# Kernel optimization log

Hardware: AMD Instinct MI355X
Metric: run time of the kernel (lower is better)

Reference implementation:

```python
import jax, jax.numpy as jnp
import numpy as np
from jax.scipy.linalg import expm

D = 12   # Fock cutoff dimension
M = 4    # qumodes per circuit
L = 2    # CVNN layers
K = M * (M - 1) // 2  # beamsplitters per interferometer
B = 1024

def _lad():
    # annihilation operator a in truncated Fock basis
    return jnp.diag(jnp.sqrt(jnp.arange(1, D, dtype=jnp.float32)), k=1).astype(jnp.complex64)

def _disp_gen(rr, ph):
    # generator of Displacement(r, phi): alpha*adag - conj(alpha)*a
    lad = _lad()
    alpha = (rr * jnp.exp(1j * ph)).astype(jnp.complex64)
    return alpha * lad.conj().T - jnp.conj(alpha) * lad

def _squeeze_mat(rr, ph):
    lad = _lad()
    z = (rr * jnp.exp(1j * ph)).astype(jnp.complex64)
    a2 = lad @ lad
    return expm(0.5 * (jnp.conj(z) * a2 - z * a2.conj().T))

def _rot_diag(ph):
    n = jnp.arange(D, dtype=jnp.float32)
    return jnp.exp(1j * ph * n).astype(jnp.complex64)

def _kerr_diag(kap):
    n = jnp.arange(D, dtype=jnp.float32)
    return jnp.exp(1j * kap * n * n).astype(jnp.complex64)

def _bs_mat(th, ph):
    # Beamsplitter exp(theta*(e^{i phi} a b^dag - e^{-i phi} a^dag b)) on D^2 space
    lad = _lad()
    eye = jnp.eye(D, dtype=jnp.complex64)
    a1 = jnp.kron(lad, eye)
    a2 = jnp.kron(eye, lad)
    H = th * (jnp.exp(1j * ph) * (a1 @ a2.conj().T) - jnp.exp(-1j * ph) * (a1.conj().T @ a2))
    return expm(H.astype(jnp.complex64)).reshape(D, D, D, D)

def _apply_1mode(psi, U, mode):
    psi = jnp.moveaxis(psi, mode + 1, -1)
    psi = psi @ U.T
    return jnp.moveaxis(psi, -1, mode + 1)

def _apply_1mode_batched(psi, U, mode):
    psi = jnp.moveaxis(psi, mode + 1, -1)
    psi = jnp.einsum('bij,b...j->b...i', U, psi)
    return jnp.moveaxis(psi, -1, mode + 1)

def _apply_diag(psi, d, mode):
    shape = [1] * psi.ndim
    shape[mode + 1] = D
    return psi * d.reshape(shape)

def _apply_2mode(psi, G, mode):
    psi = jnp.moveaxis(psi, (mode + 1, mode + 2), (-2, -1))
    psi = jnp.einsum('ijkl,...kl->...ij', G, psi)
    return jnp.moveaxis(psi, (-2, -1), (mode + 1, mode + 2))

def _interferometer(psi, theta, phi, varphi):
    # PennyLane rectangular (Clements) mesh, then per-mode rotations
    n = 0
    for ll in range(M):
        for kk in range(M - 1):
            if (ll + kk) % 2 != 1:
                psi = _apply_2mode(psi, _bs_mat(theta[n], phi[n]), kk)
                n += 1
    for m in range(M):
        psi = _apply_diag(psi, _rot_diag(varphi[m]), m)
    return psi

def _forward(x, theta_1, phi_1, varphi_1, r, phi_r, theta_2, phi_2, varphi_2, a, phi_a, k):
    b = x.shape[0]
    psi = jnp.zeros((b,) + (D,) * M, dtype=jnp.complex64)
    psi = psi.at[(slice(None),) + (0,) * M].set(1.0)  # vacuum
    # Amplitude_Phase encoding: Displacement(x[:, m], x[:, m+M]) on mode m
    for m in range(M):
        U = jax.vmap(lambda rr, ph: expm(_disp_gen(rr, ph)))(x[:, m], x[:, m + M])
        psi = _apply_1mode_batched(psi, U, m)
    # CVNeuralNetLayers
    for l in range(L):
        psi = _interferometer(psi, theta_1[l], phi_1[l], varphi_1[l])
        for m in range(M):
            psi = _apply_1mode(psi, _squeeze_mat(r[l, m], phi_r[l, m]), m)
        psi = _interferometer(psi, theta_2[l], phi_2[l], varphi_2[l])
        for m in range(M):
            psi = _apply_1mode(psi, expm(_disp_gen(a[l, m], phi_a[l, m])), m)
            psi = _apply_diag(psi, _kerr_diag(k[l, m]), m)
    # X-quadrature expvals (SF convention hbar=2: X = a + adag)
    lad = _lad()
    Xmat = lad + lad.conj().T
    sum_axes = tuple(range(1, M + 1))
    outs = [jnp.real(jnp.sum(jnp.conj(psi) * _apply_1mode(psi, Xmat, m), axis=sum_axes)) for m in range(M)]
    return jnp.stack(outs, axis=1)

def setup_inputs():
    key = jax.random.key(0)
    ks = jax.random.split(key, 12)
    tp = 2.0 * np.pi
    return {
        'x': jax.random.normal(ks[0], (B, 2 * M), dtype=jnp.float32),
        'theta_1': tp * jax.random.uniform(ks[1], (L, K), dtype=jnp.float32),
        'phi_1': tp * jax.random.uniform(ks[2], (L, K), dtype=jnp.float32),
        'varphi_1': tp * jax.random.uniform(ks[3], (L, M), dtype=jnp.float32),
        'r': 0.1 * jax.random.uniform(ks[4], (L, M), dtype=jnp.float32),
        'phi_r': tp * jax.random.uniform(ks[5], (L, M), dtype=jnp.float32),
        'theta_2': tp * jax.random.uniform(ks[6], (L, K), dtype=jnp.float32),
        'phi_2': tp * jax.random.uniform(ks[7], (L, K), dtype=jnp.float32),
        'varphi_2': tp * jax.random.uniform(ks[8], (L, M), dtype=jnp.float32),
        'a': 0.1 * jax.random.uniform(ks[9], (L, M), dtype=jnp.float32),
        'phi_a': tp * jax.random.uniform(ks[10], (L, M), dtype=jnp.float32),
        'k': tp * jax.random.uniform(ks[11], (L, M), dtype=jnp.float32),
    }

def reference(x, theta_1, phi_1, varphi_1, r, phi_r, theta_2, phi_2, varphi_2, a, phi_a, k):
    return _forward(x, theta_1, phi_1, varphi_1, r, phi_r, theta_2, phi_2, varphi_2, a, phi_a, k)
```

## Files before the change

### kernel.cpp

```cpp
#include <hip/hip_runtime.h>
#include <math.h>

#define D4 20736
#define ST 14
#define SST 168
#define KP 18

typedef float2 c32;

__device__ __forceinline__ c32 cmul(c32 a, c32 b) {
  return make_float2(a.x * b.x - a.y * b.y, a.x * b.y + a.y * b.x);
}
__device__ __forceinline__ c32 cfma(c32 a, c32 b, c32 acc) {
  acc.x = fmaf(a.x, b.x, fmaf(-a.y, b.y, acc.x));
  acc.y = fmaf(a.x, b.y, fmaf(a.y, b.x, acc.y));
  return acc;
}
__device__ __forceinline__ c32 get2(const float4* w, int n) {
  float4 q = w[n >> 1];
  return (n & 1) ? make_float2(q.z, q.w) : make_float2(q.x, q.y);
}
__device__ __forceinline__ float4 pack2(c32 a, c32 b) {
  return make_float4(a.x, a.y, b.x, b.y);
}
#define CZERO make_float2(0.f, 0.f)

__constant__ int d_secoff[24] = {0,1,5,14,30,55,91,140,204,285,385,506,650,
                                 771,871,952,1016,1065,1101,1126,1142,1151,1155,1156};

struct RM { int goff, sz, a0, da, r0, dr; };
__device__ __forceinline__ RM rmeta(int r) {
  const int i = r / 12, j = r - 12 * i, N = i + j;
  const bool up = (N <= 11);
  RM m;
  m.sz = (up ? N : 22 - N) + 1;
  const int lo = up ? 0 : (N - 11);
  m.goff = d_secoff[N] + (i - lo) * m.sz;
  m.a0 = up ? N : (143 + N);
  m.da = up ? 13 : -13;
  m.r0 = up ? N : (121 + N);
  m.dr = up ? 11 : -11;
  return m;
}

__device__ void small_expm(c32* A, c32* S, c32* P, c32* T, float* red, int sz, int tid) {
  const int n2 = sz * sz;
  if (tid < sz) {
    float s = 0.f;
    for (int j = 0; j < sz; ++j) { c32 v = A[tid * sz + j]; s += sqrtf(fmaf(v.x, v.x, v.y * v.y)); }
    red[tid] = s;
  }
  __syncthreads();
  float nrm = 0.f;
  for (int i = 0; i < sz; ++i) nrm = fmaxf(nrm, red[i]);
  int sp = 0;
  while (nrm > 0.35f && sp < 24) { nrm *= 0.5f; ++sp; }
  const float scale = ldexpf(1.f, -sp);
  for (int e = tid; e < n2; e += 64) { A[e].x *= scale; A[e].y *= scale; }
  __syncthreads();
  for (int e = tid; e < n2; e += 64) {
    c32 a = A[e];
    P[e] = a;
    if ((e / sz) == (e % sz)) a.x += 1.f;
    S[e] = a;
  }
  __syncthreads();
  for (int k = 2; k <= 12; ++k) {
    const float inv = 1.f / (float)k;
    for (int e = tid; e < n2; e += 64) {
      int i = e / sz, j = e - i * sz;
      c32 acc = CZERO;
      for (int q = 0; q < sz; ++q) acc = cfma(P[i * sz + q], A[q * sz + j], acc);
      acc.x *= inv; acc.y *= inv;
      T[e] = acc;
    }
    __syncthreads();
    for (int e = tid; e < n2; e += 64) {
      c32 t = T[e];
      P[e] = t;
      S[e].x += t.x; S[e].y += t.y;
    }
    __syncthreads();
  }
  for (int q = 0; q < sp; ++q) {
    for (int e = tid; e < n2; e += 64) {
      int i = e / sz, j = e - i * sz;
      c32 acc = CZERO;
      for (int w = 0; w < sz; ++w) acc = cfma(S[i * sz + w], S[w * sz + j], acc);
      T[e] = acc;
    }
    __syncthreads();
    for (int e = tid; e < n2; e += 64) S[e] = T[e];
    __syncthreads();
  }
}

__global__ __launch_bounds__(64) void prep_disp(const float* __restrict__ x, c32* __restrict__ c0) {
  __shared__ c32 A[144], S[144], P[144], T[144];
  __shared__ float red[12];
  const int tid = threadIdx.x;
  const int b = blockIdx.x >> 2, m = blockIdx.x & 3;
  const float rr = x[b * 8 + m], ph = x[b * 8 + 4 + m];
  float sn, cs;
  sincosf(ph, &sn, &cs);
  const c32 alpha = make_float2(rr * cs, rr * sn);
  for (int e = tid; e < 144; e += 64) A[e] = CZERO;
  __syncthreads();
  if (tid < 11) {
    float sq = sqrtf((float)(tid + 1));
    A[(tid + 1) * 12 + tid] = make_float2(alpha.x * sq, alpha.y * sq);
    A[tid * 12 + tid + 1] = make_float2(-alpha.x * sq, alpha.y * sq);
  }
  __syncthreads();
  small_expm(A, S, P, T, red, 12, tid);
  if (tid < 12) c0[(size_t)blockIdx.x * 12 + tid] = S[tid * 12];
}

__global__ __launch_bounds__(64) void prep_bs(const float* __restrict__ th1, const float* __restrict__ ph1,
                                              const float* __restrict__ th2, const float* __restrict__ ph2,
                                              c32* __restrict__ BS) {
  __shared__ c32 A[144], S[144], P[144], T[144];
  __shared__ float red[12];
  const int tid = threadIdx.x;
  const int g = blockIdx.x / 23, N = blockIdx.x % 23;
  const int l = g / 12, rem = g % 12, w = rem / 6, gi = rem % 6;
  const float th = (w ? th2 : th1)[l * 6 + gi];
  const float ph = (w ? ph2 : ph1)[l * 6 + gi];
  const int lo = (N > 11) ? (N - 11) : 0;
  const int sz = (N <= 11) ? (N + 1) : (23 - N);
  float sn, cs;
  sincosf(ph, &sn, &cs);
  for (int e = tid; e < sz * sz; e += 64) A[e] = CZERO;
  __syncthreads();
  if (tid + 1 < sz) {
    int t = tid + 1;
    float s1 = th * sqrtf((float)((lo + t) * (N - lo - t + 1)));
    A[(t - 1) * sz + t] = make_float2(cs * s1, sn * s1);
    A[t * sz + t - 1] = make_float2(-cs * s1, sn * s1);
  }
  __syncthreads();
  small_expm(A, S, P, T, red, sz, tid);
  c32* dst = BS + (size_t)g * 1156 + d_secoff[N];
  const bool upSec = (N <= 11);
  for (int e = tid; e < sz * sz; e += 64) {
    int p = e / sz, q = e - p * sz;
    int qs = upSec ? q : (sz - 1 - q);
    dst[p * sz + q] = S[p * sz + qs];
  }
}

__global__ __launch_bounds__(64) void prep_p(const float* __restrict__ r_, const float* __restrict__ phir,
                                             const float* __restrict__ vphi1,
                                             const float* __restrict__ a_, const float* __restrict__ phia,
                                             const float* __restrict__ vphi2, const float* __restrict__ kk,
                                             c32* __restrict__ P1, c32* __restrict__ P2) {
  __shared__ c32 A[144], S[144], P[144], T[144];
  __shared__ float red[12];
  const int tid = threadIdx.x;
  const int which = blockIdx.x >> 3, lm = blockIdx.x & 7;
  for (int e = tid; e < 144; e += 64) A[e] = CZERO;
  __syncthreads();
  if (which == 0) {
    const float rv = r_[lm], pv = phir[lm];
    float sn, cs;
    sincosf(pv, &sn, &cs);
    const c32 z = make_float2(rv * cs, rv * sn);
    if (tid < 10) {
      float sq = 0.5f * sqrtf((float)((tid + 1) * (tid + 2)));
      A[tid * 12 + tid + 2] = make_float2(z.x * sq, -z.y * sq);
      A[(tid + 2) * 12 + tid] = make_float2(-z.x * sq, -z.y * sq);
    }
  } else {
    const float av = a_[lm], pv = phia[lm];
    float sn, cs;
    sincosf(pv, &sn, &cs);
    const c32 alpha = make_float2(av * cs, av * sn);
    if (tid < 11) {
      float sq = sqrtf((float)(tid + 1));
      A[(tid + 1) * 12 + tid] = make_float2(alpha.x * sq, alpha.y * sq);
      A[tid * 12 + tid + 1] = make_float2(-alpha.x * sq, alpha.y * sq);
    }
  }
  __syncthreads();
  small_expm(A, S, P, T, red, 12, tid);
  if (which == 0) {
    const float vp = vphi1[lm];
    for (int e = tid; e < 144; e += 64) {
      int j = e % 12;
      float sn, cs;
      sincosf(vp * (float)j, &sn, &cs);
      P1[(size_t)lm * 144 + e] = cmul(S[e], make_float2(cs, sn));
    }
  } else {
    const float vp = vphi2[lm], kv = kk[lm];
    for (int e = tid; e < 144; e += 64) {
      int i = e / 12, j = e % 12;
      float sn1, cs1, sn2, cs2;
      sincosf(vp * (float)j, &sn1, &cs1);
      float ang = kv * (float)i;
      ang *= (float)i;
      sincosf(ang, &sn2, &cs2);
      P2[(size_t)lm * 144 + e] = cmul(make_float2(cs2, sn2), cmul(S[e], make_float2(cs1, sn1)));
    }
  }
}

__global__ __launch_bounds__(256, 5) void k123_kernel(
    c32* __restrict__ psi,
    const c32* __restrict__ gbs23, const c32* __restrict__ gbs12,
    const c32* __restrict__ gu1, const c32* __restrict__ gu2, const c32* __restrict__ gu3) {
  __shared__ __align__(16) c32 buf[2016];
  __shared__ c32 gate[1168];
  __shared__ c32 gV1[144], gV2[144], gV3[144];
  const int tid = threadIdx.x;
  if (gu1) for (int e = tid; e < 144; e += 256) gV1[e] = gu1[e];
  if (gu2) for (int e = tid; e < 144; e += 256) gV2[e] = gu2[e];
  if (gu3) for (int e = tid; e < 144; e += 256) gV3[e] = gu3[e];
  for (int e = tid; e < 1156; e += 256) gate[e] = gbs23[e];
  c32* slab = psi + (size_t)blockIdx.x * 1728;
  for (int v = tid; v < 864; v += 256) {
    float4 q = ((const float4*)slab)[v];
    *((float4*)buf + 7 * (v / 6) + (v % 6)) = q;
  }
  __syncthreads();
  const int r = tid;
  RM m;
  if (r < 144) m = rmeta(r);
  c32 acc[12];
  if (r < 144) {
#pragma unroll
    for (int n = 0; n < 12; ++n) acc[n] = CZERO;
    int a = m.a0;
#pragma unroll
    for (int t = 0; t < 12; ++t) {
      c32 g = gate[m.goff + t];
      if (t >= m.sz) g = CZERO;
#pragma unroll
      for (int n = 0; n < 12; ++n) acc[n] = cfma(g, buf[SST * n + a], acc[n]);
      a += m.da;
    }
  }
  __syncthreads();
  if (r < 144) {
    const int wr = ST * (r / 12) + (r % 12);
#pragma unroll
    for (int n = 0; n < 12; ++n) buf[SST * n + wr] = acc[n];
  }
  for (int e = tid; e < 1156; e += 256) gate[e] = gbs12[e];
  __syncthreads();
  if (r < 144) {
#pragma unroll
    for (int n = 0; n < 12; ++n) acc[n] = CZERO;
    int rho = m.r0;
#pragma unroll
    for (int t = 0; t < 12; ++t) {
      c32 g = gate[m.goff + t];
      if (t >= m.sz) g = CZERO;
      const float4* ip = (const float4*)buf + 7 * rho;
      float4 w[6];
#pragma unroll
      for (int q = 0; q < 6; ++q) w[q] = ip[q];
#pragma unroll
      for (int n = 0; n < 12; ++n) acc[n] = cfma(g, get2(w, n), acc[n]);
      rho += m.dr;
    }
  }
  __syncthreads();
  if (r < 144) {
    float4* op = (float4*)buf + 7 * r;
#pragma unroll
    for (int q = 0; q < 6; ++q) op[q] = pack2(acc[2 * q], acc[2 * q + 1]);
  }
  if (gu1) {
    __syncthreads();
    if (r < 144) {
      const int i = r / 12, n2 = r - 12 * (r / 12);
#pragma unroll
      for (int n = 0; n < 12; ++n) acc[n] = CZERO;
#pragma unroll
      for (int j = 0; j < 12; ++j) {
        c32 g = gV1[i * 12 + j];
        const float4* ip = (const float4*)buf + 7 * (12 * j + n2);
        float4 w[6];
#pragma unroll
        for (int q = 0; q < 6; ++q) w[q] = ip[q];
#pragma unroll
        for (int n = 0; n < 12; ++n) acc[n] = cfma(g, get2(w, n), acc[n]);
      }
    }
    __syncthreads();
    if (r < 144) {
      float4* op = (float4*)buf + 7 * r;
#pragma unroll
      for (int q = 0; q < 6; ++q) op[q] = pack2(acc[2 * q], acc[2 * q + 1]);
    }
  }
  if (gu2) {
    __syncthreads();
    if (r < 144) {
      const int n1 = r / 12, i = r - 12 * (r / 12);
#pragma unroll
      for (int n = 0; n < 12; ++n) acc[n] = CZERO;
#pragma unroll
      for (int j = 0; j < 12; ++j) {
        c32 g = gV2[i * 12 + j];
        const float4* ip = (const float4*)buf + 7 * (12 * n1 + j);
        float4 w[6];
#pragma unroll
        for (int q = 0; q < 6; ++q) w[q] = ip[q];
#pragma unroll
        for (int n = 0; n < 12; ++n) acc[n] = cfma(g, get2(w, n), acc[n]);
      }
    }
    __syncthreads();
    if (r < 144) {
      float4* op = (float4*)buf + 7 * r;
#pragma unroll
      for (int q = 0; q < 6; ++q) op[q] = pack2(acc[2 * q], acc[2 * q + 1]);
    }
  }
  if (gu3) {
    __syncthreads();
    if (r < 144) {
      const float4* ip = (const float4*)buf + 7 * r;
      float4 wv[6];
#pragma unroll
      for (int q = 0; q < 6; ++q) wv[q] = ip[q];
      float4* op = (float4*)buf + 7 * r;
#pragma unroll
      for (int cpair = 0; cpair < 6; ++cpair) {
        c32 s0 = CZERO, s1 = CZERO;
#pragma unroll
        for (int j = 0; j < 12; ++j) {
          c32 v = get2(wv, j);
          s0 = cfma(gV3[(2 * cpair) * 12 + j], v, s0);
          s1 = cfma(gV3[(2 * cpair + 1) * 12 + j], v, s1);
        }
        op[cpair] = pack2(s0, s1);
      }
    }
  }
  __syncthreads();
  for (int v = tid; v < 864; v += 256) {
    ((float4*)slab)[v] = *((const float4*)buf + 7 * (v / 6) + (v % 6));
  }
}

__global__ __launch_bounds__(256, 5) void k01_kernel(
    c32* __restrict__ psi, const c32* __restrict__ c0,
    const c32* __restrict__ gu0, const c32* __restrict__ gbs) {
  __shared__ __align__(16) c32 buf[2592];
  __shared__ c32 gate[1168];
  __shared__ c32 g0v[144];
  __shared__ c32 cv[4][12];
  const int tid = threadIdx.x;
  const int b = blockIdx.x / 9, t = blockIdx.x % 9;
  if (gu0) for (int e = tid; e < 144; e += 256) g0v[e] = gu0[e];
  if (gbs) for (int e = tid; e < 1156; e += 256) gate[e] = gbs[e];
  c32* gbase = psi + (size_t)b * D4 + t * 16;
  if (c0) {
    if (tid < 48) cv[tid / 12][tid % 12] = c0[(size_t)b * 48 + tid];
    __syncthreads();
    for (int e = tid; e < 2304; e += 256) {
      int row = e >> 4, q = e & 15;
      int cc = 16 * t + q, n2 = cc / 12, n3 = cc - 12 * n2;
      buf[KP * row + q] =
          cmul(cmul(cv[0][row / 12], cv[1][row % 12]), cmul(cv[2][n2], cv[3][n3]));
    }
  } else {
    for (int e = tid; e < 1152; e += 256) {
      int row = e >> 3, q = e & 7;
      ((float4*)(buf + row * KP))[q] = ((const float4*)(gbase + (size_t)row * 144))[q];
    }
  }
  __syncthreads();
  const int r = tid;
  c32 acc[16];
  if (gu0) {
    if (r < 144) {
      const int i = r / 12, n1 = r - 12 * (r / 12);
#pragma unroll
      for (int n = 0; n < 16; ++n) acc[n] = CZERO;
#pragma unroll
      for (int j = 0; j < 12; ++j) {
        c32 g = g0v[i * 12 + j];
        const float4* ip = (const float4*)(buf + (12 * j + n1) * KP);
        float4 w[8];
#pragma unroll
        for (int q = 0; q < 8; ++q) w[q] = ip[q];
#pragma unroll
        for (int n = 0; n < 16; ++n) acc[n] = cfma(g, get2(w, n), acc[n]);
      }
    }
    __syncthreads();
    if (r < 144) {
      float4* op = (float4*)(buf + r * KP);
#pragma unroll
      for (int q = 0; q < 8; ++q) op[q] = pack2(acc[2 * q], acc[2 * q + 1]);
    }
    __syncthreads();
  }
  if (gbs) {
    if (r < 144) {
      const RM m = rmeta(r);
#pragma unroll
      for (int n = 0; n < 16; ++n) acc[n] = CZERO;
      int rho = m.r0;
#pragma unroll
      for (int tk = 0; tk < 12; ++tk) {
        c32 g = gate[m.goff + tk];
        if (tk >= m.sz) g = CZERO;
        const float4* ip = (const float4*)(buf + rho * KP);
        float4 w[8];
#pragma unroll
        for (int q = 0; q < 8; ++q) w[q] = ip[q];
#pragma unroll
        for (int n = 0; n < 16; ++n) acc[n] = cfma(g, get2(w, n), acc[n]);
        rho += m.dr;
      }
    }
    __syncthreads();
    if (r < 144) {
      float4* op = (float4*)(buf + r * KP);
#pragma unroll
      for (int q = 0; q < 8; ++q) op[q] = pack2(acc[2 * q], acc[2 * q + 1]);
    }
    __syncthreads();
  }
  for (int e = tid; e < 1152; e += 256) {
    int row = e >> 3, q = e & 7;
    ((float4*)(gbase + (size_t)row * 144))[q] = ((const float4*)(buf + row * KP))[q];
  }
}

__global__ __launch_bounds__(256) void expval_kernel(const c32* __restrict__ psi, float* __restrict__ out) {
  __shared__ float red[1024];
  __shared__ float sq2[12];
  const int tid = threadIdx.x, b = blockIdx.x;
  if (tid < 12) sq2[tid] = 2.f * sqrtf((float)(tid + 1));
  __syncthreads();
  const c32* base = psi + (size_t)b * D4;
  float a0 = 0.f, a1 = 0.f, a2 = 0.f, a3 = 0.f;
  for (int e = tid; e < D4; e += 256) {
    c32 p = base[e];
    int n3 = e % 12, t = e / 12;
    int n2 = t % 12; t /= 12;
    int n1 = t % 12, n0 = t / 12;
    if (n3 < 11) { c32 q = base[e + 1];    a3 = fmaf(sq2[n3], fmaf(p.x, q.x, p.y * q.y), a3); }
    if (n2 < 11) { c32 q = base[e + 12];   a2 = fmaf(sq2[n2], fmaf(p.x, q.x, p.y * q.y), a2); }
    if (n1 < 11) { c32 q = base[e + 144];  a1 = fmaf(sq2[n1], fmaf(p.x, q.x, p.y * q.y), a1); }
    if (n0 < 11) { c32 q = base[e + 1728]; a0 = fmaf(sq2[n0], fmaf(p.x, q.x, p.y * q.y), a0); }
  }
  red[tid * 4 + 0] = a0; red[tid * 4 + 1] = a1; red[tid * 4 + 2] = a2; red[tid * 4 + 3] = a3;
  __syncthreads();
  for (int s = 128; s > 0; s >>= 1) {
    if (tid < s) {
      red[tid * 4 + 0] += red[(tid + s) * 4 + 0];
      red[tid * 4 + 1] += red[(tid + s) * 4 + 1];
      red[tid * 4 + 2] += red[(tid + s) * 4 + 2];
      red[tid * 4 + 3] += red[(tid + s) * 4 + 3];
    }
    __syncthreads();
  }
  if (tid < 4) out[b * 4 + tid] = red[tid];
}

extern "C" void kernel_launch(void* const* d_in, const int* in_sizes, int n_in,
                              void* d_out, int out_size, void* d_ws, size_t ws_size,
                              hipStream_t stream) {
  const float* x      = (const float*)d_in[0];
  const float* theta1 = (const float*)d_in[1];
  const float* phi1   = (const float*)d_in[2];
  const float* vphi1  = (const float*)d_in[3];
  const float* r_     = (const float*)d_in[4];
  const float* phir   = (const float*)d_in[5];
  const float* theta2 = (const float*)d_in[6];
  const float* phi2   = (const float*)d_in[7];
  const float* vphi2  = (const float*)d_in[8];
  const float* a_     = (const float*)d_in[9];
  const float* phia   = (const float*)d_in[10];
  const float* kk     = (const float*)d_in[11];
  float* out = (float*)d_out;

  const size_t PSI_OFF = 0;
  const size_t C0_OFF  = 169869312;
  const size_t P1_OFF  = C0_OFF + 393216;
  const size_t P2_OFF  = P1_OFF + 9216;
  const size_t BS_OFF  = P2_OFF + 9216;
  const size_t NEED    = BS_OFF + 221952;
  if (ws_size < NEED) return;

  char* ws = (char*)d_ws;
  c32* psi = (c32*)(ws + PSI_OFF);
  c32* c0  = (c32*)(ws + C0_OFF);
  c32* P1  = (c32*)(ws + P1_OFF);
  c32* P2  = (c32*)(ws + P2_OFF);
  c32* BS  = (c32*)(ws + BS_OFF);

  prep_disp<<<dim3(4096), dim3(64), 0, stream>>>(x, c0);
  prep_bs<<<dim3(552), dim3(64), 0, stream>>>(theta1, phi1, theta2, phi2, BS);
  prep_p<<<dim3(16), dim3(64), 0, stream>>>(r_, phir, vphi1, a_, phia, vphi2, kk, P1, P2);

  for (int l = 0; l < 2; ++l) {
    c32* bsl = BS + (size_t)l * 12 * 1156;
    const c32* c0arg = (l == 0) ? c0 : (const c32*)nullptr;
    const c32* u0pre = (l == 0) ? (const c32*)nullptr : (const c32*)(P2 + (size_t)(l - 1) * 4 * 144);
    k01_kernel<<<dim3(9216), dim3(256), 0, stream>>>(psi, c0arg, u0pre, bsl + 0 * 1156);
    k123_kernel<<<dim3(12288), dim3(256), 0, stream>>>(psi, bsl + 1 * 1156, bsl + 2 * 1156,
                                                       nullptr, nullptr, nullptr);
    k01_kernel<<<dim3(9216), dim3(256), 0, stream>>>(psi, nullptr, nullptr, bsl + 3 * 1156);
    k123_kernel<<<dim3(12288), dim3(256), 0, stream>>>(psi, bsl + 4 * 1156, bsl + 5 * 1156,
                                                       P1 + (size_t)(l * 4 + 1) * 144,
                                                       P1 + (size_t)(l * 4 + 2) * 144,
                                                       P1 + (size_t)(l * 4 + 3) * 144);
    k01_kernel<<<dim3(9216), dim3(256), 0, stream>>>(psi, nullptr, P1 + (size_t)(l * 4 + 0) * 144, bsl + 6 * 1156);
    k123_kernel<<<dim3(12288), dim3(256), 0, stream>>>(psi, bsl + 7 * 1156, bsl + 8 * 1156,
                                                       nullptr, nullptr, nullptr);
    k01_kernel<<<dim3(9216), dim3(256), 0, stream>>>(psi, nullptr, nullptr, bsl + 9 * 1156);
    k123_kernel<<<dim3(12288), dim3(256), 0, stream>>>(psi, bsl + 10 * 1156, bsl + 11 * 1156,
                                                       P2 + (size_t)(l * 4 + 1) * 144,
                                                       P2 + (size_t)(l * 4 + 2) * 144,
                                                       P2 + (size_t)(l * 4 + 3) * 144);
  }
  k01_kernel<<<dim3(9216), dim3(256), 0, stream>>>(psi, nullptr, P2 + (size_t)(1 * 4 + 0) * 144, nullptr);
  expval_kernel<<<dim3(1024), dim3(256), 0, stream>>>(psi, out);
}
```

Baseline: 2.182 ms.

## Skip zero beamsplitter taps and sort rows by sector size to balance waves

The beamsplitter stages now loop only over the real sector size per output row instead of a fixed 12 taps with zero-masked gates. A permutation table assigns rows to threads so that rows with similar sector sizes share a wavefront, which cuts divergence. The gate tables are stored transposed so each thread strides through them. Single-mode unitaries move into the padding columns of the psi buffer, the second beamsplitter gate is prefetched into registers, and the kernel's occupancy target goes from 5 to 6 blocks per SM. The price is a dynamic loop bound in place of full unrolling and more register pressure from the prefetch.

```diff
diff --git a/kernel.cpp b/kernel.cpp
--- a/kernel.cpp
+++ b/kernel.cpp
@@ -27,6 +27,32 @@
 
 __constant__ int d_secoff[24] = {0,1,5,14,30,55,91,140,204,285,385,506,650,
                                  771,871,952,1016,1065,1101,1126,1142,1151,1155,1156};
+
+__constant__ unsigned char d_perm[144] = {
+  11,22,33,44,55,66,77,88,99,110,121,132,
+  10,21,32,43,54,65,76,87,98,109,120,
+  23,34,45,56,67,78,89,100,111,122,133,
+  9,20,31,42,53,64,75,86,97,108,
+  35,46,57,68,79,90,101,112,123,134,
+  8,19,30,41,52,63,74,85,96,
+  47,58,69,80,91,102,113,124,135,
+  7,18,29,40,51,62,73,84,
+  59,70,81,92,103,114,125,136,
+  6,17,28,39,50,61,72,
+  71,82,93,104,115,126,137,
+  5,16,27,38,49,60,
+  83,94,105,116,127,138,
+  4,15,26,37,48,
+  95,106,117,128,139,
+  3,14,25,36,
+  107,118,129,140,
+  2,13,24,
+  119,130,141,
+  1,12,
+  131,142,
+  0,
+  143
+};
 
 struct RM { int goff, sz, a0, da, r0, dr; };
 __device__ __forceinline__ RM rmeta(int r) {
@@ -35,7 +61,7 @@
   RM m;
   m.sz = (up ? N : 22 - N) + 1;
   const int lo = up ? 0 : (N - 11);
-  m.goff = d_secoff[N] + (i - lo) * m.sz;
+  m.goff = d_secoff[N] + (i - lo);
   m.a0 = up ? N : (143 + N);
   m.da = up ? 13 : -13;
   m.r0 = up ? N : (121 + N);
@@ -145,7 +171,7 @@
   for (int e = tid; e < sz * sz; e += 64) {
     int p = e / sz, q = e - p * sz;
     int qs = upSec ? q : (sz - 1 - q);
-    dst[p * sz + q] = S[p * sz + qs];
+    dst[q * sz + p] = S[p * sz + qs];
   }
 }
 
@@ -205,17 +231,22 @@
   }
 }
 
-__global__ __launch_bounds__(256, 5) void k123_kernel(
+__global__ __launch_bounds__(256, 6) void k123_kernel(
     c32* __restrict__ psi,
     const c32* __restrict__ gbs23, const c32* __restrict__ gbs12,
     const c32* __restrict__ gu1, const c32* __restrict__ gu2, const c32* __restrict__ gu3) {
   __shared__ __align__(16) c32 buf[2016];
   __shared__ c32 gate[1168];
-  __shared__ c32 gV1[144], gV2[144], gV3[144];
   const int tid = threadIdx.x;
-  if (gu1) for (int e = tid; e < 144; e += 256) gV1[e] = gu1[e];
-  if (gu2) for (int e = tid; e < 144; e += 256) gV2[e] = gu2[e];
-  if (gu3) for (int e = tid; e < 144; e += 256) gV3[e] = gu3[e];
+  c32 pf[5];
+#pragma unroll
+  for (int k = 0; k < 5; ++k) {
+    int e = tid + 256 * k;
+    pf[k] = (e < 1156) ? gbs12[e] : CZERO;
+  }
+  c32 pf3 = (gu3 && tid < 144) ? gu3[tid] : CZERO;
+  if (gu1) for (int e = tid; e < 144; e += 256) buf[ST * e + 12] = gu1[e];
+  if (gu2) for (int e = tid; e < 144; e += 256) buf[ST * e + 13] = gu2[e];
   for (int e = tid; e < 1156; e += 256) gate[e] = gbs23[e];
   c32* slab = psi + (size_t)blockIdx.x * 1728;
   for (int v = tid; v < 864; v += 256) {
@@ -223,39 +254,41 @@
     *((float4*)buf + 7 * (v / 6) + (v % 6)) = q;
   }
   __syncthreads();
-  const int r = tid;
+  const int rb = (tid < 144) ? (int)d_perm[tid] : 0;
   RM m;
-  if (r < 144) m = rmeta(r);
+  if (tid < 144) m = rmeta(rb);
   c32 acc[12];
-  if (r < 144) {
+  if (tid < 144) {
 #pragma unroll
     for (int n = 0; n < 12; ++n) acc[n] = CZERO;
-    int a = m.a0;
-#pragma unroll
-    for (int t = 0; t < 12; ++t) {
-      c32 g = gate[m.goff + t];
-      if (t >= m.sz) g = CZERO;
+    int a = m.a0, go = m.goff;
+    for (int t = 0; t < m.sz; ++t) {
+      c32 g = gate[go];
+      go += m.sz;
 #pragma unroll
       for (int n = 0; n < 12; ++n) acc[n] = cfma(g, buf[SST * n + a], acc[n]);
       a += m.da;
     }
   }
   __syncthreads();
-  if (r < 144) {
-    const int wr = ST * (r / 12) + (r % 12);
+  if (tid < 144) {
+    const int wr = ST * (rb / 12) + (rb % 12);
 #pragma unroll
     for (int n = 0; n < 12; ++n) buf[SST * n + wr] = acc[n];
   }
-  for (int e = tid; e < 1156; e += 256) gate[e] = gbs12[e];
-  __syncthreads();
-  if (r < 144) {
+#pragma unroll
+  for (int k = 0; k < 5; ++k) {
+    int e = tid + 256 * k;
+    if (e < 1156) gate[e] = pf[k];
+  }
+  __syncthreads();
+  if (tid < 144) {
 #pragma unroll
     for (int n = 0; n < 12; ++n) acc[n] = CZERO;
-    int rho = m.r0;
-#pragma unroll
-    for (int t = 0; t < 12; ++t) {
-      c32 g = gate[m.goff + t];
-      if (t >= m.sz) g = CZERO;
+    int rho = m.r0, go = m.goff;
+    for (int t = 0; t < m.sz; ++t) {
+      c32 g = gate[go];
+      go += m.sz;
       const float4* ip = (const float4*)buf + 7 * rho;
       float4 w[6];
 #pragma unroll
@@ -266,20 +299,21 @@
     }
   }
   __syncthreads();
-  if (r < 144) {
-    float4* op = (float4*)buf + 7 * r;
+  if (tid < 144) {
+    float4* op = (float4*)buf + 7 * rb;
 #pragma unroll
     for (int q = 0; q < 6; ++q) op[q] = pack2(acc[2 * q], acc[2 * q + 1]);
   }
+  if (gu3 && tid < 144) gate[tid] = pf3;
   if (gu1) {
     __syncthreads();
-    if (r < 144) {
-      const int i = r / 12, n2 = r - 12 * (r / 12);
+    if (tid < 144) {
+      const int i = tid / 12, n2 = tid - 12 * (tid / 12);
 #pragma unroll
       for (int n = 0; n < 12; ++n) acc[n] = CZERO;
 #pragma unroll
       for (int j = 0; j < 12; ++j) {
-        c32 g = gV1[i * 12 + j];
+        c32 g = buf[ST * (i * 12 + j) + 12];
         const float4* ip = (const float4*)buf + 7 * (12 * j + n2);
         float4 w[6];
 #pragma unroll
@@ -289,21 +323,21 @@
       }
     }
     __syncthreads();
-    if (r < 144) {
-      float4* op = (float4*)buf + 7 * r;
+    if (tid < 144) {
+      float4* op = (float4*)buf + 7 * tid;
 #pragma unroll
       for (int q = 0; q < 6; ++q) op[q] = pack2(acc[2 * q], acc[2 * q + 1]);
     }
   }
   if (gu2) {
     __syncthreads();
-    if (r < 144) {
-      const int n1 = r / 12, i = r - 12 * (r / 12);
+    if (tid < 144) {
+      const int n1 = tid / 12, i = tid - 12 * (tid / 12);
 #pragma unroll
       for (int n = 0; n < 12; ++n) acc[n] = CZERO;
 #pragma unroll
       for (int j = 0; j < 12; ++j) {
-        c32 g = gV2[i * 12 + j];
+        c32 g = buf[ST * (i * 12 + j) + 13];
         const float4* ip = (const float4*)buf + 7 * (12 * n1 + j);
         float4 w[6];
 #pragma unroll
@@ -313,28 +347,28 @@
       }
     }
     __syncthreads();
-    if (r < 144) {
-      float4* op = (float4*)buf + 7 * r;
+    if (tid < 144) {
+      float4* op = (float4*)buf + 7 * tid;
 #pragma unroll
       for (int q = 0; q < 6; ++q) op[q] = pack2(acc[2 * q], acc[2 * q + 1]);
     }
   }
   if (gu3) {
     __syncthreads();
-    if (r < 144) {
-      const float4* ip = (const float4*)buf + 7 * r;
+    if (tid < 144) {
+      const float4* ip = (const float4*)buf + 7 * tid;
       float4 wv[6];
 #pragma unroll
       for (int q = 0; q < 6; ++q) wv[q] = ip[q];
-      float4* op = (float4*)buf + 7 * r;
+      float4* op = (float4*)buf + 7 * tid;
 #pragma unroll
       for (int cpair = 0; cpair < 6; ++cpair) {
         c32 s0 = CZERO, s1 = CZERO;
 #pragma unroll
         for (int j = 0; j < 12; ++j) {
           c32 v = get2(wv, j);
-          s0 = cfma(gV3[(2 * cpair) * 12 + j], v, s0);
-          s1 = cfma(gV3[(2 * cpair + 1) * 12 + j], v, s1);
+          s0 = cfma(gate[(2 * cpair) * 12 + j], v, s0);
+          s1 = cfma(gate[(2 * cpair + 1) * 12 + j], v, s1);
         }
         op[cpair] = pack2(s0, s1);
       }
@@ -351,11 +385,10 @@
     const c32* __restrict__ gu0, const c32* __restrict__ gbs) {
   __shared__ __align__(16) c32 buf[2592];
   __shared__ c32 gate[1168];
-  __shared__ c32 g0v[144];
   __shared__ c32 cv[4][12];
   const int tid = threadIdx.x;
   const int b = blockIdx.x / 9, t = blockIdx.x % 9;
-  if (gu0) for (int e = tid; e < 144; e += 256) g0v[e] = gu0[e];
+  if (gu0) for (int e = tid; e < 144; e += 256) buf[KP * e + 16] = gu0[e];
   if (gbs) for (int e = tid; e < 1156; e += 256) gate[e] = gbs[e];
   c32* gbase = psi + (size_t)b * D4 + t * 16;
   if (c0) {
@@ -374,16 +407,15 @@
     }
   }
   __syncthreads();
-  const int r = tid;
   c32 acc[16];
   if (gu0) {
-    if (r < 144) {
-      const int i = r / 12, n1 = r - 12 * (r / 12);
+    if (tid < 144) {
+      const int i = tid / 12, n1 = tid - 12 * (tid / 12);
 #pragma unroll
       for (int n = 0; n < 16; ++n) acc[n] = CZERO;
 #pragma unroll
       for (int j = 0; j < 12; ++j) {
-        c32 g = g0v[i * 12 + j];
+        c32 g = buf[(i * 12 + j) * KP + 16];
         const float4* ip = (const float4*)(buf + (12 * j + n1) * KP);
         float4 w[8];
 #pragma unroll
@@ -393,23 +425,23 @@
       }
     }
     __syncthreads();
-    if (r < 144) {
-      float4* op = (float4*)(buf + r * KP);
+    if (tid < 144) {
+      float4* op = (float4*)(buf + tid * KP);
 #pragma unroll
       for (int q = 0; q < 8; ++q) op[q] = pack2(acc[2 * q], acc[2 * q + 1]);
     }
     __syncthreads();
   }
   if (gbs) {
-    if (r < 144) {
-      const RM m = rmeta(r);
+    const int rb = (tid < 144) ? (int)d_perm[tid] : 0;
+    if (tid < 144) {
+      const RM m = rmeta(rb);
 #pragma unroll
       for (int n = 0; n < 16; ++n) acc[n] = CZERO;
-      int rho = m.r0;
-#pragma unroll
-      for (int tk = 0; tk < 12; ++tk) {
-        c32 g = gate[m.goff + tk];
-        if (tk >= m.sz) g = CZERO;
+      int rho = m.r0, go = m.goff;
+      for (int tk = 0; tk < m.sz; ++tk) {
+        c32 g = gate[go];
+        go += m.sz;
         const float4* ip = (const float4*)(buf + rho * KP);
         float4 w[8];
 #pragma unroll
@@ -420,8 +452,8 @@
       }
     }
     __syncthreads();
-    if (r < 144) {
-      float4* op = (float4*)(buf + r * KP);
+    if (tid < 144) {
+      float4* op = (float4*)(buf + rb * KP);
 #pragma unroll
       for (int q = 0; q < 8; ++q) op[q] = pack2(acc[2 * q], acc[2 * q + 1]);
     }
```

Result: faster. 2.059 ms (-5.6%).
